# Optimization experiments

Hardware: AMD Instinct MI355X
Metric: run time of the kernel (lower is better)

Reference implementation:

```python
import jax, jax.numpy as jnp
import numpy as np

B, N, F_IN = 32, 512, 16
H, D_HID, D_OUT = 8, 8, 32
ALPHA = 0.2
NEG = -9e15


def setup_inputs() -> dict:
    key = jax.random.key(0)
    ks = jax.random.split(key, 10)
    xv = jax.random.normal(ks[0], (B, N, F_IN), dtype=jnp.float32)
    adj = (jax.random.uniform(ks[1], (B, N, N)) < 0.05).astype(jnp.float32)
    s = 0.1
    W_heads = jax.random.normal(ks[2], (H, F_IN, D_HID), dtype=jnp.float32) * s
    a1 = jax.random.normal(ks[3], (H, D_HID), dtype=jnp.float32) * s
    a2 = jax.random.normal(ks[4], (H, D_HID), dtype=jnp.float32) * s
    W_out = jax.random.normal(ks[5], (H * D_HID, D_OUT), dtype=jnp.float32) * s
    a1_out = jax.random.normal(ks[6], (D_OUT,), dtype=jnp.float32) * s
    a2_out = jax.random.normal(ks[7], (D_OUT,), dtype=jnp.float32) * s
    W_q = jax.random.normal(ks[8], (N * D_OUT, N), dtype=jnp.float32) * s
    b_q = jax.random.normal(ks[9], (N,), dtype=jnp.float32) * s
    return {"xv": xv, "adj": adj, "W_heads": W_heads, "a1": a1, "a2": a2,
            "W_out": W_out, "a1_out": a1_out, "a2_out": a2_out,
            "W_q": W_q, "b_q": b_q}


def _masked_softmax(e, adj_mask):
    # e: [..., N, N]; adj_mask broadcastable bool
    scores = jnp.where(adj_mask, e, NEG)
    return jax.nn.softmax(scores, axis=-1)


def reference(xv, adj, W_heads, a1, a2, W_out, a1_out, a2_out, W_q, b_q):
    mask = adj > 0  # [B, N, N]
    # --- multi-head GAT layer (vectorized over batch and heads) ---
    Wh = jnp.einsum('bnf,hfd->bhnd', xv, W_heads)            # [B,H,N,Dh]
    f1 = jnp.einsum('bhnd,hd->bhn', Wh, a1)                   # a^T[:Dh] . Wh_i
    f2 = jnp.einsum('bhnd,hd->bhn', Wh, a2)                   # a^T[Dh:] . Wh_j
    e = jax.nn.leaky_relu(f1[:, :, :, None] + f2[:, :, None, :], ALPHA)  # [B,H,N,N]
    att = _masked_softmax(e, mask[:, None, :, :])
    h = jnp.einsum('bhnm,bhmd->bhnd', att, Wh)
    h = jax.nn.elu(h)                                         # concat=True heads apply elu
    h_cat = jnp.transpose(h, (0, 2, 1, 3)).reshape(B, N, H * D_HID)  # head-major concat
    # --- output attention layer (concat=False: no internal elu) ---
    Who = jnp.einsum('bnf,fd->bnd', h_cat, W_out)             # [B,N,Do]
    g1 = Who @ a1_out                                         # [B,N]
    g2 = Who @ a2_out
    eo = jax.nn.leaky_relu(g1[:, :, None] + g2[:, None, :], ALPHA)
    att_o = _masked_softmax(eo, mask)
    out = jnp.einsum('bnm,bmd->bnd', att_o, Who)
    out = jax.nn.elu(out)                                     # F.elu applied in forward
    # --- Q head ---
    q = out.reshape(B, N * D_OUT) @ W_q + b_q                 # [B,N]
    return q[..., None]                                       # [B,N,1]
```

## Files before the change

### kernel.cpp

```cpp
#include <hip/hip_runtime.h>
#include <stdint.h>


typedef unsigned long long u64;

__device__ __forceinline__ float eluf(float x) { return x > 0.f ? x : __expf(x) - 1.f; }
__device__ __forceinline__ float lrelu(float x) { return fmaxf(x, 0.2f * x); }

__device__ u64   g_mask[131072];
__device__ float g_hcat[1048576];
__device__ float g_Who[524288];
__device__ float g_g1[16384];
__device__ float g_g2[16384];
__device__ float g_out2[524288];
__device__ float g_partial[4194304];

__global__ __launch_bounds__(256) void k_mask(const float* __restrict__ adj) {
  int wid = blockIdx.x * 4 + (threadIdx.x >> 6);
  int lane = threadIdx.x & 63;
#pragma unroll
  for (int seg = 0; seg < 16; ++seg) {
    int gw = wid * 16 + seg;
    float v = adj[(size_t)(gw >> 3) * 512 + (gw & 7) * 64 + lane];
    u64 bal = __ballot(v > 0.f);
    if (lane == 0) g_mask[gw] = bal;
  }
}

__global__ __launch_bounds__(512) void k_gat(const float* __restrict__ xv,
                                             const float* __restrict__ whd,
                                             const float* __restrict__ a1,
                                             const float* __restrict__ a2) {
  __shared__ float w_s[128];
  __shared__ float a1s[8], a2s[8];
  __shared__ float sm[4608];

  int bh = blockIdx.x;
  int b = bh >> 3, h = bh & 7;
  int tid = threadIdx.x;

  const u64* mrow = g_mask + (size_t)b * 4096 + (size_t)tid * 8;
  u64 mreg[8];
#pragma unroll
  for (int w = 0; w < 8; ++w) mreg[w] = mrow[w];

  if (tid < 128) w_s[tid] = whd[h * 128 + tid];
  if (tid < 8) { a1s[tid] = a1[h * 8 + tid]; a2s[tid] = a2[h * 8 + tid]; }
  __syncthreads();

  const float4* xp = (const float4*)(xv + (size_t)(b * 512 + tid) * 16);
  float x[16];
#pragma unroll
  for (int i = 0; i < 4; ++i) {
    float4 v = xp[i];
    x[4 * i] = v.x; x[4 * i + 1] = v.y; x[4 * i + 2] = v.z; x[4 * i + 3] = v.w;
  }
  float wh[8] = {0, 0, 0, 0, 0, 0, 0, 0};
#pragma unroll
  for (int f = 0; f < 16; ++f) {
    float xf = x[f];
#pragma unroll
    for (int d = 0; d < 8; ++d) wh[d] += xf * w_s[f * 8 + d];
  }
  float f1v = 0.f, s2 = 0.f;
#pragma unroll
  for (int d = 0; d < 8; ++d) { f1v += wh[d] * a1s[d]; s2 += wh[d] * a2s[d]; }
#pragma unroll
  for (int d = 0; d < 8; ++d) sm[d * 512 + tid] = wh[d];
  sm[4096 + tid] = s2;
  __syncthreads();

  float acc[8] = {0, 0, 0, 0, 0, 0, 0, 0};
  float sum = 0.f;
#pragma unroll
  for (int g = 0; g < 4; ++g) {
    u64 m0 = mreg[2 * g], m1 = mreg[2 * g + 1];
    while (m0 | m1) {
      bool use0 = (m0 != 0);
      u64 cur = use0 ? m0 : m1;
      int j = __builtin_ctzll(cur);
      u64 nxt = cur & (cur - 1);
      m0 = use0 ? nxt : m0;
      m1 = use0 ? m1 : nxt;
      int col = g * 128 + (use0 ? 0 : 64) + j;
      float p = __expf(lrelu(f1v + sm[4096 + col]));
      sum += p;
      acc[0] += p * sm[col];
      acc[1] += p * sm[512 + col];
      acc[2] += p * sm[1024 + col];
      acc[3] += p * sm[1536 + col];
      acc[4] += p * sm[2048 + col];
      acc[5] += p * sm[2560 + col];
      acc[6] += p * sm[3072 + col];
      acc[7] += p * sm[3584 + col];
    }
  }

  float rs = sum > 0.f ? 1.0f / sum : 0.f;
  float* dst = g_hcat + (size_t)(b * 512 + tid) * 64 + h * 8;
  *(float4*)dst = make_float4(eluf(acc[0] * rs), eluf(acc[1] * rs), eluf(acc[2] * rs), eluf(acc[3] * rs));
  *(float4*)(dst + 4) = make_float4(eluf(acc[4] * rs), eluf(acc[5] * rs), eluf(acc[6] * rs), eluf(acc[7] * rs));
}

__global__ __launch_bounds__(128) void k_who(const float* __restrict__ wout,
                                             const float* __restrict__ a1o,
                                             const float* __restrict__ a2o) {
  __shared__ float wo_s[2048];
  __shared__ float a1s[32], a2s[32];
  int tid = threadIdx.x;
  for (int i = tid; i < 2048; i += 128) wo_s[i] = wout[i];
  if (tid < 32) { a1s[tid] = a1o[tid]; a2s[tid] = a2o[tid]; }
  __syncthreads();

  int idx = blockIdx.x * 128 + tid;
  int g = idx >> 1;
  int db = (idx & 1) * 16;

  const float4* hp = (const float4*)(g_hcat + (size_t)g * 64);
  float acc[16];
#pragma unroll
  for (int d = 0; d < 16; ++d) acc[d] = 0.f;
#pragma unroll
  for (int f4 = 0; f4 < 16; ++f4) {
    float4 h4 = hp[f4];
    float hv[4] = {h4.x, h4.y, h4.z, h4.w};
#pragma unroll
    for (int k = 0; k < 4; ++k) {
      const float* wr = wo_s + (f4 * 4 + k) * 32 + db;
      float hvk = hv[k];
#pragma unroll
      for (int d = 0; d < 16; ++d) acc[d] += hvk * wr[d];
    }
  }
  float s1 = 0.f, s2 = 0.f;
#pragma unroll
  for (int d = 0; d < 16; ++d) { s1 += acc[d] * a1s[db + d]; s2 += acc[d] * a2s[db + d]; }
  s1 += __shfl_xor(s1, 1);
  s2 += __shfl_xor(s2, 1);

  float* wdst = g_Who + (size_t)g * 32 + db;
#pragma unroll
  for (int d4 = 0; d4 < 4; ++d4)
    *(float4*)(wdst + d4 * 4) = make_float4(acc[d4 * 4], acc[d4 * 4 + 1], acc[d4 * 4 + 2], acc[d4 * 4 + 3]);
  if ((idx & 1) == 0) { g_g1[g] = s1; g_g2[g] = s2; }
}

__global__ __launch_bounds__(512) void k_att2() {
  __shared__ float pool[9472];
  __shared__ u64 mask_s[512];

  int b = blockIdx.x >> 3;
  int t = blockIdx.x & 7;
  int tid = threadIdx.x;
  int w = tid >> 6;
  int l = tid & 63;

  mask_s[tid] = g_mask[(size_t)b * 4096 + t * 512 + tid];
  float g1v = g_g1[(size_t)b * 512 + t * 64 + l];

  float acc[32];
#pragma unroll
  for (int d = 0; d < 32; ++d) acc[d] = 0.f;
  float sum = 0.f;

#pragma unroll 1
  for (int c = 0; c < 2; ++c) {
    __syncthreads();
    {
      for (int i = tid; i < 2048; i += 512) {
        int m = i & 255, dg = i >> 8;
        float4 v = *(const float4*)(g_Who + (size_t)(b * 512 + c * 256 + m) * 32 + dg * 4);
        pool[(dg * 4 + 0) * 256 + m] = v.x;
        pool[(dg * 4 + 1) * 256 + m] = v.y;
        pool[(dg * 4 + 2) * 256 + m] = v.z;
        pool[(dg * 4 + 3) * 256 + m] = v.w;
      }
      if (tid < 64) ((float4*)(pool + 9216))[tid] = ((const float4*)g_g2)[(size_t)b * 128 + c * 64 + tid];
    }
    __syncthreads();
    u64 mq = mask_s[l * 8 + c * 4 + (w >> 1)];
    uint32_t bits = (w & 1) ? (uint32_t)(mq >> 32) : (uint32_t)mq;
    while (bits) {
      int j = __builtin_ctz(bits);
      bits &= bits - 1;
      int col = w * 32 + j;
      float p = __expf(lrelu(g1v + pool[9216 + col]));
      sum += p;
#pragma unroll
      for (int d = 0; d < 32; ++d) acc[d] += p * pool[d * 256 + col];
    }
  }

#pragma unroll 1
  for (int step = 4; step >= 1; step >>= 1) {
    __syncthreads();
    if (w >= step && w < 2 * step) {
      float* rp = pool + (size_t)((w - step) * 64 + l) * 36;
#pragma unroll
      for (int d4 = 0; d4 < 8; ++d4)
        *(float4*)(rp + d4 * 4) = make_float4(acc[d4 * 4], acc[d4 * 4 + 1], acc[d4 * 4 + 2], acc[d4 * 4 + 3]);
      rp[32] = sum;
    }
    __syncthreads();
    if (w < step) {
      const float* rp = pool + (size_t)(w * 64 + l) * 36;
#pragma unroll
      for (int d = 0; d < 32; ++d) acc[d] += rp[d];
      sum += rp[32];
    }
  }

  if (w == 0) {
    float rs = sum > 0.f ? 1.0f / sum : 0.f;
    float* dst = g_out2 + (size_t)(b * 512 + t * 64 + l) * 32;
#pragma unroll
    for (int d4 = 0; d4 < 8; ++d4)
      *(float4*)(dst + d4 * 4) = make_float4(eluf(acc[d4 * 4] * rs), eluf(acc[d4 * 4 + 1] * rs),
                                             eluf(acc[d4 * 4 + 2] * rs), eluf(acc[d4 * 4 + 3] * rs));
  }
}

__global__ __launch_bounds__(512) void k_qpart(const float* __restrict__ Wq) {
  __shared__ float outS[64 * 36];
  int s = blockIdx.x >> 1;
  int c = blockIdx.x & 1;
  int tid = threadIdx.x;
  int lane = tid & 63;
  int bg = tid >> 6;

  if (tid < 512) {
    int i = tid;
    int bb = i >> 4, kk4 = (i & 15) * 4;
    float4 v = *(const float4*)(g_out2 + (size_t)bb * 16384 + s * 64 + kk4);
    outS[(kk4 + 0) * 36 + bb] = v.x;
    outS[(kk4 + 1) * 36 + bb] = v.y;
    outS[(kk4 + 2) * 36 + bb] = v.z;
    outS[(kk4 + 3) * 36 + bb] = v.w;
  }
  __syncthreads();

  const float* wp = Wq + (size_t)(s * 64) * 512 + c * 256 + lane * 4;
  float4 acc[4];
#pragma unroll
  for (int j = 0; j < 4; ++j) acc[j] = make_float4(0.f, 0.f, 0.f, 0.f);

#pragma unroll 8
  for (int kk = 0; kk < 64; ++kk) {
    float4 wv = *(const float4*)(wp + (size_t)kk * 512);
    const float* ob = outS + kk * 36 + bg * 4;
    float4 o = *(const float4*)(ob);
    float ov[4] = {o.x, o.y, o.z, o.w};
#pragma unroll
    for (int j = 0; j < 4; ++j) {
      acc[j].x += ov[j] * wv.x; acc[j].y += ov[j] * wv.y;
      acc[j].z += ov[j] * wv.z; acc[j].w += ov[j] * wv.w;
    }
  }
#pragma unroll
  for (int j = 0; j < 4; ++j)
    *(float4*)(g_partial + (size_t)(s * 32 + bg * 4 + j) * 512 + c * 256 + lane * 4) = acc[j];
}

__global__ __launch_bounds__(256) void k_qred(const float* __restrict__ bq,
                                              float* __restrict__ out) {
  __shared__ float red[4][64];
  int tid = threadIdx.x;
  int w = tid >> 6, lane = tid & 63;
  int g = blockIdx.x * 64 + lane;
  int b = g >> 9, np = g & 511;

  float q = 0.f;
#pragma unroll 8
  for (int i = 0; i < 64; ++i) {
    int s = w + i * 4;
    q += g_partial[(size_t)(s * 32 + b) * 512 + np];
  }
  red[w][lane] = q;
  __syncthreads();
  if (w == 0)
    out[g] = bq[np] + red[0][lane] + red[1][lane] + red[2][lane] + red[3][lane];
}

extern "C" void kernel_launch(void* const* d_in, const int* in_sizes, int n_in,
                              void* d_out, int out_size, void* d_ws, size_t ws_size,
                              hipStream_t stream) {
  const float* xv = (const float*)d_in[0];
  const float* adj = (const float*)d_in[1];
  const float* W_heads = (const float*)d_in[2];
  const float* a1 = (const float*)d_in[3];
  const float* a2 = (const float*)d_in[4];
  const float* W_out = (const float*)d_in[5];
  const float* a1_out = (const float*)d_in[6];
  const float* a2_out = (const float*)d_in[7];
  const float* W_q = (const float*)d_in[8];
  const float* b_q = (const float*)d_in[9];

  k_mask<<<2048, 256, 0, stream>>>(adj);
  k_gat<<<256, 512, 0, stream>>>(xv, W_heads, a1, a2);
  k_who<<<256, 128, 0, stream>>>(W_out, a1_out, a2_out);
  k_att2<<<256, 512, 0, stream>>>();
  k_qpart<<<512, 512, 0, stream>>>(W_q);
  k_qred<<<256, 256, 0, stream>>>(b_q, (float*)d_out);
}
```

Baseline: 171.5 us.

## Restructure second attention, stage Wq in LDS, and pack head features

The second attention kernel changes from splitting columns across warps with an LDS tree reduction to assigning each node row to 8 threads, each owning 4 output dims. Every thread walks the full adjacency bitmask against a padded transposed Who tile held in LDS, so the cross-warp reduction and its syncs go away. The Q-projection kernel now stages Wq tiles in shared memory and splits K into 128-chunks, which halves the partial buffer and the reduction depth. The first GAT kernel stores head features as float2 pairs to cut LDS load count. The trade-off is that the mask-walk loop is repeated by 8 threads per row and the kernel uses more LDS.

```diff
diff --git a/kernel.cpp b/kernel.cpp
--- a/kernel.cpp
+++ b/kernel.cpp
@@ -13,7 +13,7 @@
 __device__ float g_g1[16384];
 __device__ float g_g2[16384];
 __device__ float g_out2[524288];
-__device__ float g_partial[4194304];
+__device__ float g_partial[2097152];
 
 __global__ __launch_bounds__(256) void k_mask(const float* __restrict__ adj) {
   int wid = blockIdx.x * 4 + (threadIdx.x >> 6);
@@ -33,7 +33,8 @@
                                              const float* __restrict__ a2) {
   __shared__ float w_s[128];
   __shared__ float a1s[8], a2s[8];
-  __shared__ float sm[4608];
+  __shared__ float whp[4104];
+  __shared__ float f2s[512];
 
   int bh = blockIdx.x;
   int b = bh >> 3, h = bh & 7;
@@ -65,9 +66,10 @@
   float f1v = 0.f, s2 = 0.f;
 #pragma unroll
   for (int d = 0; d < 8; ++d) { f1v += wh[d] * a1s[d]; s2 += wh[d] * a2s[d]; }
-#pragma unroll
-  for (int d = 0; d < 8; ++d) sm[d * 512 + tid] = wh[d];
-  sm[4096 + tid] = s2;
+  f2s[tid] = s2;
+#pragma unroll
+  for (int d2 = 0; d2 < 4; ++d2)
+    *(float2*)(whp + d2 * 1026 + tid * 2) = make_float2(wh[2 * d2], wh[2 * d2 + 1]);
   __syncthreads();
 
   float acc[8] = {0, 0, 0, 0, 0, 0, 0, 0};
@@ -83,16 +85,14 @@
       m0 = use0 ? nxt : m0;
       m1 = use0 ? m1 : nxt;
       int col = g * 128 + (use0 ? 0 : 64) + j;
-      float p = __expf(lrelu(f1v + sm[4096 + col]));
+      float p = __expf(lrelu(f1v + f2s[col]));
       sum += p;
-      acc[0] += p * sm[col];
-      acc[1] += p * sm[512 + col];
-      acc[2] += p * sm[1024 + col];
-      acc[3] += p * sm[1536 + col];
-      acc[4] += p * sm[2048 + col];
-      acc[5] += p * sm[2560 + col];
-      acc[6] += p * sm[3072 + col];
-      acc[7] += p * sm[3584 + col];
+      float2 A = *(const float2*)(whp + col * 2);
+      float2 Bv = *(const float2*)(whp + 1026 + col * 2);
+      float2 C = *(const float2*)(whp + 2052 + col * 2);
+      float2 D = *(const float2*)(whp + 3078 + col * 2);
+      acc[0] += p * A.x;  acc[1] += p * A.y;  acc[2] += p * Bv.x; acc[3] += p * Bv.y;
+      acc[4] += p * C.x;  acc[5] += p * C.y;  acc[6] += p * D.x;  acc[7] += p * D.y;
     }
   }
 
@@ -146,92 +146,81 @@
 }
 
 __global__ __launch_bounds__(512) void k_att2() {
-  __shared__ float pool[9472];
-  __shared__ u64 mask_s[512];
+  __shared__ float whoT[16416];
+  __shared__ float g2s[512];
 
   int b = blockIdx.x >> 3;
   int t = blockIdx.x & 7;
   int tid = threadIdx.x;
-  int w = tid >> 6;
-  int l = tid & 63;
-
-  mask_s[tid] = g_mask[(size_t)b * 4096 + t * 512 + tid];
-  float g1v = g_g1[(size_t)b * 512 + t * 64 + l];
-
-  float acc[32];
-#pragma unroll
-  for (int d = 0; d < 32; ++d) acc[d] = 0.f;
-  float sum = 0.f;
-
-#pragma unroll 1
-  for (int c = 0; c < 2; ++c) {
-    __syncthreads();
-    {
-      for (int i = tid; i < 2048; i += 512) {
-        int m = i & 255, dg = i >> 8;
-        float4 v = *(const float4*)(g_Who + (size_t)(b * 512 + c * 256 + m) * 32 + dg * 4);
-        pool[(dg * 4 + 0) * 256 + m] = v.x;
-        pool[(dg * 4 + 1) * 256 + m] = v.y;
-        pool[(dg * 4 + 2) * 256 + m] = v.z;
-        pool[(dg * 4 + 3) * 256 + m] = v.w;
-      }
-      if (tid < 64) ((float4*)(pool + 9216))[tid] = ((const float4*)g_g2)[(size_t)b * 128 + c * 64 + tid];
+  int l = tid >> 3;
+  int dg = tid & 7;
+  int row = t * 64 + l;
+
+  const u64* mrow = g_mask + (size_t)b * 4096 + (size_t)row * 8;
+  u64 mreg[8];
+#pragma unroll
+  for (int w = 0; w < 8; ++w) mreg[w] = mrow[w];
+  float g1v = g_g1[(size_t)b * 512 + row];
+
+  for (int i = tid; i < 4096; i += 512) {
+    int col = i >> 3, dgi = i & 7;
+    float4 v = *(const float4*)(g_Who + (size_t)(b * 512 + col) * 32 + dgi * 4);
+    whoT[(dgi * 4 + 0) * 513 + col] = v.x;
+    whoT[(dgi * 4 + 1) * 513 + col] = v.y;
+    whoT[(dgi * 4 + 2) * 513 + col] = v.z;
+    whoT[(dgi * 4 + 3) * 513 + col] = v.w;
+  }
+  g2s[tid] = g_g2[(size_t)b * 512 + tid];
+  __syncthreads();
+
+  const float* wp0 = whoT + (dg * 4 + 0) * 513;
+  const float* wp1 = whoT + (dg * 4 + 1) * 513;
+  const float* wp2 = whoT + (dg * 4 + 2) * 513;
+  const float* wp3 = whoT + (dg * 4 + 3) * 513;
+
+  float a0 = 0.f, a1v = 0.f, a2v = 0.f, a3 = 0.f, sum = 0.f;
+#pragma unroll
+  for (int g = 0; g < 4; ++g) {
+    u64 m0 = mreg[2 * g], m1 = mreg[2 * g + 1];
+    while (m0 | m1) {
+      bool use0 = (m0 != 0);
+      u64 cur = use0 ? m0 : m1;
+      int j = __builtin_ctzll(cur);
+      u64 nxt = cur & (cur - 1);
+      m0 = use0 ? nxt : m0;
+      m1 = use0 ? m1 : nxt;
+      int col = g * 128 + (use0 ? 0 : 64) + j;
+      float p = __expf(lrelu(g1v + g2s[col]));
+      sum += p;
+      a0 += p * wp0[col];
+      a1v += p * wp1[col];
+      a2v += p * wp2[col];
+      a3 += p * wp3[col];
     }
-    __syncthreads();
-    u64 mq = mask_s[l * 8 + c * 4 + (w >> 1)];
-    uint32_t bits = (w & 1) ? (uint32_t)(mq >> 32) : (uint32_t)mq;
-    while (bits) {
-      int j = __builtin_ctz(bits);
-      bits &= bits - 1;
-      int col = w * 32 + j;
-      float p = __expf(lrelu(g1v + pool[9216 + col]));
-      sum += p;
-#pragma unroll
-      for (int d = 0; d < 32; ++d) acc[d] += p * pool[d * 256 + col];
-    }
-  }
-
-#pragma unroll 1
-  for (int step = 4; step >= 1; step >>= 1) {
-    __syncthreads();
-    if (w >= step && w < 2 * step) {
-      float* rp = pool + (size_t)((w - step) * 64 + l) * 36;
-#pragma unroll
-      for (int d4 = 0; d4 < 8; ++d4)
-        *(float4*)(rp + d4 * 4) = make_float4(acc[d4 * 4], acc[d4 * 4 + 1], acc[d4 * 4 + 2], acc[d4 * 4 + 3]);
-      rp[32] = sum;
-    }
-    __syncthreads();
-    if (w < step) {
-      const float* rp = pool + (size_t)(w * 64 + l) * 36;
-#pragma unroll
-      for (int d = 0; d < 32; ++d) acc[d] += rp[d];
-      sum += rp[32];
-    }
-  }
-
-  if (w == 0) {
-    float rs = sum > 0.f ? 1.0f / sum : 0.f;
-    float* dst = g_out2 + (size_t)(b * 512 + t * 64 + l) * 32;
-#pragma unroll
-    for (int d4 = 0; d4 < 8; ++d4)
-      *(float4*)(dst + d4 * 4) = make_float4(eluf(acc[d4 * 4] * rs), eluf(acc[d4 * 4 + 1] * rs),
-                                             eluf(acc[d4 * 4 + 2] * rs), eluf(acc[d4 * 4 + 3] * rs));
-  }
+  }
+
+  float rs = sum > 0.f ? 1.0f / sum : 0.f;
+  *(float4*)(g_out2 + (size_t)(b * 512 + row) * 32 + dg * 4) =
+      make_float4(eluf(a0 * rs), eluf(a1v * rs), eluf(a2v * rs), eluf(a3 * rs));
 }
 
 __global__ __launch_bounds__(512) void k_qpart(const float* __restrict__ Wq) {
-  __shared__ float outS[64 * 36];
-  int s = blockIdx.x >> 1;
-  int c = blockIdx.x & 1;
+  __shared__ float wqS[16384];
+  __shared__ float outS[4608];
+  int s = blockIdx.x >> 2;
+  int c = blockIdx.x & 3;
   int tid = threadIdx.x;
   int lane = tid & 63;
   int bg = tid >> 6;
 
-  if (tid < 512) {
-    int i = tid;
-    int bb = i >> 4, kk4 = (i & 15) * 4;
-    float4 v = *(const float4*)(g_out2 + (size_t)bb * 16384 + s * 64 + kk4);
+  for (int i = tid; i < 4096; i += 512) {
+    int kk = i >> 5, n4 = i & 31;
+    *(float4*)(wqS + kk * 128 + n4 * 4) =
+        *(const float4*)(Wq + (size_t)(s * 128 + kk) * 512 + c * 128 + n4 * 4);
+  }
+  for (int i = tid; i < 1024; i += 512) {
+    int bb = i >> 5, kk4 = (i & 31) * 4;
+    float4 v = *(const float4*)(g_out2 + (size_t)bb * 16384 + s * 128 + kk4);
     outS[(kk4 + 0) * 36 + bb] = v.x;
     outS[(kk4 + 1) * 36 + bb] = v.y;
     outS[(kk4 + 2) * 36 + bb] = v.z;
@@ -239,26 +228,22 @@
   }
   __syncthreads();
 
-  const float* wp = Wq + (size_t)(s * 64) * 512 + c * 256 + lane * 4;
-  float4 acc[4];
-#pragma unroll
-  for (int j = 0; j < 4; ++j) acc[j] = make_float4(0.f, 0.f, 0.f, 0.f);
+  float2 acc[4];
+#pragma unroll
+  for (int j = 0; j < 4; ++j) acc[j] = make_float2(0.f, 0.f);
 
 #pragma unroll 8
-  for (int kk = 0; kk < 64; ++kk) {
-    float4 wv = *(const float4*)(wp + (size_t)kk * 512);
-    const float* ob = outS + kk * 36 + bg * 4;
-    float4 o = *(const float4*)(ob);
-    float ov[4] = {o.x, o.y, o.z, o.w};
-#pragma unroll
-    for (int j = 0; j < 4; ++j) {
-      acc[j].x += ov[j] * wv.x; acc[j].y += ov[j] * wv.y;
-      acc[j].z += ov[j] * wv.z; acc[j].w += ov[j] * wv.w;
-    }
+  for (int kk = 0; kk < 128; ++kk) {
+    float2 wv = *(const float2*)(wqS + kk * 128 + lane * 2);
+    const float4 o = *(const float4*)(outS + kk * 36 + bg * 4);
+    acc[0].x += o.x * wv.x; acc[0].y += o.x * wv.y;
+    acc[1].x += o.y * wv.x; acc[1].y += o.y * wv.y;
+    acc[2].x += o.z * wv.x; acc[2].y += o.z * wv.y;
+    acc[3].x += o.w * wv.x; acc[3].y += o.w * wv.y;
   }
 #pragma unroll
   for (int j = 0; j < 4; ++j)
-    *(float4*)(g_partial + (size_t)(s * 32 + bg * 4 + j) * 512 + c * 256 + lane * 4) = acc[j];
+    *(float2*)(g_partial + (size_t)(s * 32 + bg * 4 + j) * 512 + c * 128 + lane * 2) = acc[j];
 }
 
 __global__ __launch_bounds__(256) void k_qred(const float* __restrict__ bq,
@@ -271,7 +256,7 @@
 
   float q = 0.f;
 #pragma unroll 8
-  for (int i = 0; i < 64; ++i) {
+  for (int i = 0; i < 32; ++i) {
     int s = w + i * 4;
     q += g_partial[(size_t)(s * 32 + b) * 512 + np];
   }
```

Result: no change. 170.3 us (-0.7%).
